# Performance work log

Hardware: AMD Instinct MI355X
Metric: run time of the kernel (lower is better)

The kernel has to match this reference:

```python
import jax, jax.numpy as jnp
import numpy as np

NUM_FRAMES = 4  # camera, person, object, world
RELATION_DIM = 14
CANONICAL_DIM = 64
BATCH = 2097152


def setup_inputs() -> dict:
    key = jax.random.key(0)
    k1, k2, k3, k4 = jax.random.split(key, 4)
    relation_logits = jax.random.normal(k1, (BATCH, RELATION_DIM), dtype=jnp.float32)
    frame_type_ids = jax.random.randint(k2, (BATCH,), 0, NUM_FRAMES, dtype=jnp.int32)
    # stacked per-frame-type Linear params: W[k] is (out=64, in=14), b[k] is (64,)
    bound = 1.0 / np.sqrt(RELATION_DIM)
    W = jax.random.uniform(k3, (NUM_FRAMES, CANONICAL_DIM, RELATION_DIM), dtype=jnp.float32,
                           minval=-bound, maxval=bound)
    b = jax.random.uniform(k4, (NUM_FRAMES, CANONICAL_DIM), dtype=jnp.float32,
                           minval=-bound, maxval=bound)
    return {"relation_logits": relation_logits, "frame_type_ids": frame_type_ids,
            "W": W, "b": b}


def reference(relation_logits, frame_type_ids, W, b):
    # Per-frame-type linear routing: out[i] = x[i] @ W[id_i].T + b[id_i].
    # Loop over the 4 small experts (fixed structural set), masked-select outputs.
    batch = relation_logits.shape[0]
    out = jnp.zeros((batch, W.shape[1]), dtype=relation_logits.dtype)
    for k in range(W.shape[0]):
        yk = relation_logits @ W[k].T + b[k]          # (batch, canonical_dim)
        sel = (frame_type_ids == k)[:, None]
        out = jnp.where(sel, yk, out)
    return out
```

## Files before the change

### kernel.cpp

```cpp
#include <hip/hip_runtime.h>
#include <stdint.h>

#define RDIM 14
#define CDIM 64
#define NFRAMES 4

constexpr int BLOCK = 256;
constexpr int TILE_ROWS = 256;
constexpr int ROWS_PER_WAVE = 64;
constexpr int X_TILE_BYTES = TILE_ROWS * RDIM * 4;
constexpr int CHUNK_BYTES  = 64 * 16;
constexpr int N_CHUNKS     = X_TILE_BYTES / CHUNK_BYTES;

typedef const __attribute__((address_space(1))) uint32_t* gptr_t;
typedef __attribute__((address_space(3))) uint32_t* lptr_t;

__global__ __launch_bounds__(BLOCK, 4) void frame_proj_kernel(
    const float* __restrict__ X,
    const int* __restrict__ ids,
    const float* __restrict__ W,
    const float* __restrict__ B,
    float* __restrict__ out,
    int batch)
{
    __shared__ float xs_lds[TILE_ROWS * RDIM];

    const int tid  = threadIdx.x;
    const int lane = tid & 63;
    const int wid  = __builtin_amdgcn_readfirstlane(tid >> 6);

    const int tileBase = blockIdx.x * TILE_ROWS;
    const int tileRows = min(TILE_ROWS, batch - tileBase);

    const int waveRow0 = wid * ROWS_PER_WAVE;
    const int gRow0    = tileBase + waveRow0;
    int idv = 0;
    if (gRow0 + lane < batch) idv = ids[gRow0 + lane];

    if (tileRows == TILE_ROWS) {
        const char* gsrc = (const char*)(X + (size_t)tileBase * RDIM);
        for (int c = wid; c < N_CHUNKS; c += 4) {
            __builtin_amdgcn_global_load_lds(
                (gptr_t)(const void*)(gsrc + c * CHUNK_BYTES + lane * 16),
                (lptr_t)(void*)((char*)xs_lds + c * CHUNK_BYTES),
                16, 0, 0);
        }
    } else {
        for (int i = tid; i < tileRows * RDIM; i += BLOCK)
            xs_lds[i] = X[(size_t)tileBase * RDIM + i];
    }

    float w[NFRAMES][RDIM];
    float bb[NFRAMES];
#pragma unroll
    for (int e = 0; e < NFRAMES; ++e) {
#pragma unroll
        for (int k = 0; k < RDIM; ++k)
            w[e][k] = W[(e * CDIM + lane) * RDIM + k];
        bb[e] = B[e * CDIM + lane];
    }
#pragma unroll
    for (int e = 0; e < NFRAMES; ++e) {
#pragma unroll
        for (int k = 0; k < RDIM; ++k)
            asm volatile("" : "+v"(w[e][k]));
        asm volatile("" : "+v"(bb[e]));
    }

    __syncthreads();

    const int nrows = min(ROWS_PER_WAVE, tileRows - waveRow0);
    const float2* xr = (const float2*)xs_lds + waveRow0 * (RDIM / 2);
    float* orow = out + (size_t)gRow0 * CDIM + lane;

    for (int r = 0; r < nrows; ++r) {
        const int id = __builtin_amdgcn_readlane(idv, r);

        float xv[RDIM];
#pragma unroll
        for (int k = 0; k < RDIM / 2; ++k) {
            float2 v = xr[r * (RDIM / 2) + k];
            xv[2 * k]     = v.x;
            xv[2 * k + 1] = v.y;
        }

        auto dot = [&](const float (&wk)[RDIM], float bias) {
            float a0 = bias, a1 = 0.0f;
#pragma unroll
            for (int k = 0; k < RDIM; k += 2) {
                a0 = fmaf(xv[k],     wk[k],     a0);
                a1 = fmaf(xv[k + 1], wk[k + 1], a1);
            }
            return a0 + a1;
        };

        float acc;
        if (id == 0)      acc = dot(w[0], bb[0]);
        else if (id == 1) acc = dot(w[1], bb[1]);
        else if (id == 2) acc = dot(w[2], bb[2]);
        else              acc = dot(w[3], bb[3]);

        orow[(size_t)r * CDIM] = acc;
    }
}

extern "C" void kernel_launch(void* const* d_in, const int* in_sizes, int n_in,
                              void* d_out, int out_size, void* d_ws, size_t ws_size,
                              hipStream_t stream) {
    const float* X   = (const float*)d_in[0];
    const int*   ids = (const int*)d_in[1];
    const float* W   = (const float*)d_in[2];
    const float* B   = (const float*)d_in[3];
    float* out = (float*)d_out;

    const int batch = in_sizes[1];

    const int grid = (batch + TILE_ROWS - 1) / TILE_ROWS;
    frame_proj_kernel<<<grid, BLOCK, 0, stream>>>(X, ids, W, B, out, batch);
}
```

Before: 617.3 us.

## Double tile rows and pad LDS rows to 16 floats for float4 reads

Tile size grows from 256 to 512 rows, so each wave handles 128 rows and needs two id registers. Each 14-float input row is now staged into a 16-float padded slot in LDS using per-lane 16-byte global_load_lds chunks, which lets the inner loop read a row with four float4 LDS loads instead of seven float2 loads. The full-tile loop is also unrolled by two. The intent is to cut LDS instruction count and amortize the weight loads over more rows. The risk is that the 16-byte chunks past float 14 read into the next row's data, which is why the fast path now requires a following tile to exist, and the larger LDS footprint reduces occupancy.

```diff
diff --git a/kernel.cpp b/kernel.cpp
--- a/kernel.cpp
+++ b/kernel.cpp
@@ -6,11 +6,13 @@
 #define NFRAMES 4
 
 constexpr int BLOCK = 256;
-constexpr int TILE_ROWS = 256;
-constexpr int ROWS_PER_WAVE = 64;
-constexpr int X_TILE_BYTES = TILE_ROWS * RDIM * 4;
-constexpr int CHUNK_BYTES  = 64 * 16;
-constexpr int N_CHUNKS     = X_TILE_BYTES / CHUNK_BYTES;
+constexpr int TILE_ROWS = 512;
+constexpr int ROWS_PER_WAVE = TILE_ROWS / 4;
+constexpr int ROW_PAD_FLOATS = 16;
+constexpr int X_TILE_BYTES = TILE_ROWS * ROW_PAD_FLOATS * 4;
+constexpr int CHUNK_BYTES = 16;
+constexpr int N_CHUNKS = X_TILE_BYTES / CHUNK_BYTES;
+constexpr int ISSUES = N_CHUNKS / 64;
 
 typedef const __attribute__((address_space(1))) uint32_t* gptr_t;
 typedef __attribute__((address_space(3))) uint32_t* lptr_t;
@@ -23,7 +25,7 @@
     float* __restrict__ out,
     int batch)
 {
-    __shared__ float xs_lds[TILE_ROWS * RDIM];
+    __shared__ float xs_lds[TILE_ROWS * ROW_PAD_FLOATS];
 
     const int tid  = threadIdx.x;
     const int lane = tid & 63;
@@ -34,73 +36,85 @@
 
     const int waveRow0 = wid * ROWS_PER_WAVE;
     const int gRow0    = tileBase + waveRow0;
-    int idv = 0;
-    if (gRow0 + lane < batch) idv = ids[gRow0 + lane];
+    int idv0 = 0, idv1 = 0;
+    if (gRow0 + lane < batch)      idv0 = ids[gRow0 + lane];
+    if (gRow0 + 64 + lane < batch) idv1 = ids[gRow0 + 64 + lane];
 
-    if (tileRows == TILE_ROWS) {
+    if (tileBase + TILE_ROWS < batch) {
         const char* gsrc = (const char*)(X + (size_t)tileBase * RDIM);
-        for (int c = wid; c < N_CHUNKS; c += 4) {
+        for (int i = wid; i < ISSUES; i += 4) {
+            const int c = i * 64 + lane;
+            const int r = c >> 2;
+            const int q = c & 3;
             __builtin_amdgcn_global_load_lds(
-                (gptr_t)(const void*)(gsrc + c * CHUNK_BYTES + lane * 16),
-                (lptr_t)(void*)((char*)xs_lds + c * CHUNK_BYTES),
+                (gptr_t)(const void*)(gsrc + r * 56 + q * 16),
+                (lptr_t)(void*)((char*)xs_lds + i * 1024),
                 16, 0, 0);
         }
     } else {
-        for (int i = tid; i < tileRows * RDIM; i += BLOCK)
-            xs_lds[i] = X[(size_t)tileBase * RDIM + i];
+        for (int i = tid; i < tileRows * ROW_PAD_FLOATS; i += BLOCK) {
+            const int r = i >> 4, k = i & 15;
+            xs_lds[i] = (k < RDIM) ? X[(size_t)(tileBase + r) * RDIM + k] : 0.0f;
+        }
     }
 
-    float w[NFRAMES][RDIM];
-    float bb[NFRAMES];
+    float2 w2[NFRAMES][7];
+    float  bb[NFRAMES];
 #pragma unroll
     for (int e = 0; e < NFRAMES; ++e) {
+        const float2* wr = (const float2*)(W + (size_t)(e * CDIM + lane) * RDIM);
 #pragma unroll
-        for (int k = 0; k < RDIM; ++k)
-            w[e][k] = W[(e * CDIM + lane) * RDIM + k];
+        for (int k = 0; k < 7; ++k) w2[e][k] = wr[k];
         bb[e] = B[e * CDIM + lane];
     }
 #pragma unroll
     for (int e = 0; e < NFRAMES; ++e) {
 #pragma unroll
-        for (int k = 0; k < RDIM; ++k)
-            asm volatile("" : "+v"(w[e][k]));
+        for (int k = 0; k < 7; ++k) asm volatile("" : "+v"(w2[e][k]));
         asm volatile("" : "+v"(bb[e]));
     }
 
     __syncthreads();
 
     const int nrows = min(ROWS_PER_WAVE, tileRows - waveRow0);
-    const float2* xr = (const float2*)xs_lds + waveRow0 * (RDIM / 2);
+    const float4* xr4 = (const float4*)xs_lds + (size_t)waveRow0 * 4;
     float* orow = out + (size_t)gRow0 * CDIM + lane;
 
-    for (int r = 0; r < nrows; ++r) {
-        const int id = __builtin_amdgcn_readlane(idv, r);
+    auto body = [&](int r) {
+        const int id = (r < 64) ? __builtin_amdgcn_readlane(idv0, r & 63)
+                                : __builtin_amdgcn_readlane(idv1, r & 63);
 
-        float xv[RDIM];
+        float4 v0 = xr4[r * 4 + 0];
+        float4 v1 = xr4[r * 4 + 1];
+        float4 v2 = xr4[r * 4 + 2];
+        float4 v3 = xr4[r * 4 + 3];
+        float2 x2[7] = { {v0.x, v0.y}, {v0.z, v0.w}, {v1.x, v1.y}, {v1.z, v1.w},
+                         {v2.x, v2.y}, {v2.z, v2.w}, {v3.x, v3.y} };
+
+        auto dot = [&](const float2 (&wk)[7], float bias) {
+            float ax = bias, ay = 0.0f;
 #pragma unroll
-        for (int k = 0; k < RDIM / 2; ++k) {
-            float2 v = xr[r * (RDIM / 2) + k];
-            xv[2 * k]     = v.x;
-            xv[2 * k + 1] = v.y;
-        }
-
-        auto dot = [&](const float (&wk)[RDIM], float bias) {
-            float a0 = bias, a1 = 0.0f;
-#pragma unroll
-            for (int k = 0; k < RDIM; k += 2) {
-                a0 = fmaf(xv[k],     wk[k],     a0);
-                a1 = fmaf(xv[k + 1], wk[k + 1], a1);
+            for (int k = 0; k < 7; ++k) {
+                ax = fmaf(x2[k].x, wk[k].x, ax);
+                ay = fmaf(x2[k].y, wk[k].y, ay);
             }
-            return a0 + a1;
+            return ax + ay;
         };
 
         float acc;
-        if (id == 0)      acc = dot(w[0], bb[0]);
-        else if (id == 1) acc = dot(w[1], bb[1]);
-        else if (id == 2) acc = dot(w[2], bb[2]);
-        else              acc = dot(w[3], bb[3]);
+        if (id == 0)      acc = dot(w2[0], bb[0]);
+        else if (id == 1) acc = dot(w2[1], bb[1]);
+        else if (id == 2) acc = dot(w2[2], bb[2]);
+        else              acc = dot(w2[3], bb[3]);
 
         orow[(size_t)r * CDIM] = acc;
+    };
+
+    if (nrows == ROWS_PER_WAVE) {
+#pragma unroll 2
+        for (int r = 0; r < ROWS_PER_WAVE; ++r) body(r);
+    } else {
+        for (int r = 0; r < nrows; ++r) body(r);
     }
 }
 
```

Result: slower. 675.0 us (+9.3%).

## Make projection kernel persistent with double-buffered LDS prefetch of input tiles

Applied to the files above, without the earlier changes.

The grid is capped at a fixed number of persistent blocks that loop over tiles. Each block prefetches the next tile's X rows into a second LDS buffer and loads the next ids while computing the current tile. The goal is to overlap input loads with compute and stores, and to pay the per-block weight register load only once. This doubles LDS use, which may cut occupancy, and adds a block barrier per tile. It also reads weights as float2.

```diff
diff --git a/kernel.cpp b/kernel.cpp
--- a/kernel.cpp
+++ b/kernel.cpp
@@ -8,9 +8,11 @@
 constexpr int BLOCK = 256;
 constexpr int TILE_ROWS = 256;
 constexpr int ROWS_PER_WAVE = 64;
-constexpr int X_TILE_BYTES = TILE_ROWS * RDIM * 4;
-constexpr int CHUNK_BYTES  = 64 * 16;
-constexpr int N_CHUNKS     = X_TILE_BYTES / CHUNK_BYTES;
+constexpr int X_TILE_FLOATS = TILE_ROWS * RDIM;
+constexpr int X_TILE_BYTES  = X_TILE_FLOATS * 4;
+constexpr int CHUNK_BYTES   = 64 * 16;
+constexpr int N_CHUNKS      = X_TILE_BYTES / CHUNK_BYTES;
+constexpr int PERSISTENT_BLOCKS = 1024;
 
 typedef const __attribute__((address_space(1))) uint32_t* gptr_t;
 typedef __attribute__((address_space(3))) uint32_t* lptr_t;
@@ -23,84 +25,112 @@
     float* __restrict__ out,
     int batch)
 {
-    __shared__ float xs_lds[TILE_ROWS * RDIM];
+    __shared__ float xs[2][X_TILE_FLOATS];
 
     const int tid  = threadIdx.x;
     const int lane = tid & 63;
     const int wid  = __builtin_amdgcn_readfirstlane(tid >> 6);
+    const int waveRow0 = wid * ROWS_PER_WAVE;
 
-    const int tileBase = blockIdx.x * TILE_ROWS;
-    const int tileRows = min(TILE_ROWS, batch - tileBase);
+    const int ntiles = (batch + TILE_ROWS - 1) / TILE_ROWS;
 
-    const int waveRow0 = wid * ROWS_PER_WAVE;
-    const int gRow0    = tileBase + waveRow0;
-    int idv = 0;
-    if (gRow0 + lane < batch) idv = ids[gRow0 + lane];
+    auto stage = [&](int tile, int buf) {
+        const int tb = tile * TILE_ROWS;
+        const int trows = min(TILE_ROWS, batch - tb);
+        if (trows == TILE_ROWS) {
+            const char* gsrc = (const char*)(X + (size_t)tb * RDIM);
+            for (int c = wid; c < N_CHUNKS; c += 4) {
+                __builtin_amdgcn_global_load_lds(
+                    (gptr_t)(const void*)(gsrc + c * CHUNK_BYTES + lane * 16),
+                    (lptr_t)(void*)((char*)xs[buf] + c * CHUNK_BYTES),
+                    16, 0, 0);
+            }
+        } else {
+            for (int i = tid; i < trows * RDIM; i += BLOCK)
+                xs[buf][i] = X[(size_t)tb * RDIM + i];
+        }
+    };
 
-    if (tileRows == TILE_ROWS) {
-        const char* gsrc = (const char*)(X + (size_t)tileBase * RDIM);
-        for (int c = wid; c < N_CHUNKS; c += 4) {
-            __builtin_amdgcn_global_load_lds(
-                (gptr_t)(const void*)(gsrc + c * CHUNK_BYTES + lane * 16),
-                (lptr_t)(void*)((char*)xs_lds + c * CHUNK_BYTES),
-                16, 0, 0);
-        }
-    } else {
-        for (int i = tid; i < tileRows * RDIM; i += BLOCK)
-            xs_lds[i] = X[(size_t)tileBase * RDIM + i];
-    }
+    auto load_ids = [&](int tile) -> int {
+        const int g = tile * TILE_ROWS + waveRow0 + lane;
+        return (g < batch) ? ids[g] : 0;
+    };
+
+    int t = blockIdx.x;
+    if (t >= ntiles) return;
+
+    stage(t, 0);
+    int idv = load_ids(t);
 
     float w[NFRAMES][RDIM];
     float bb[NFRAMES];
 #pragma unroll
     for (int e = 0; e < NFRAMES; ++e) {
+        const float2* wr = (const float2*)(W + (size_t)(e * CDIM + lane) * RDIM);
 #pragma unroll
-        for (int k = 0; k < RDIM; ++k)
-            w[e][k] = W[(e * CDIM + lane) * RDIM + k];
+        for (int k = 0; k < 7; ++k) {
+            float2 v = wr[k];
+            w[e][2 * k]     = v.x;
+            w[e][2 * k + 1] = v.y;
+        }
         bb[e] = B[e * CDIM + lane];
     }
 #pragma unroll
     for (int e = 0; e < NFRAMES; ++e) {
 #pragma unroll
-        for (int k = 0; k < RDIM; ++k)
-            asm volatile("" : "+v"(w[e][k]));
+        for (int k = 0; k < RDIM; ++k) asm volatile("" : "+v"(w[e][k]));
         asm volatile("" : "+v"(bb[e]));
     }
 
     __syncthreads();
 
-    const int nrows = min(ROWS_PER_WAVE, tileRows - waveRow0);
-    const float2* xr = (const float2*)xs_lds + waveRow0 * (RDIM / 2);
-    float* orow = out + (size_t)gRow0 * CDIM + lane;
+    int cur = 0;
+    while (true) {
+        const int tn = t + gridDim.x;
+        const bool havenext = (tn < ntiles);
+        if (havenext) stage(tn, cur ^ 1);
+        const int idv_next = havenext ? load_ids(tn) : 0;
 
-    for (int r = 0; r < nrows; ++r) {
-        const int id = __builtin_amdgcn_readlane(idv, r);
+        const int tb = t * TILE_ROWS;
+        const int nrows = min(ROWS_PER_WAVE, batch - tb - waveRow0);
+        const float2* xr2 = (const float2*)(xs[cur]) + waveRow0 * (RDIM / 2);
+        float* orow = out + (size_t)(tb + waveRow0) * CDIM + lane;
 
-        float xv[RDIM];
+        for (int r = 0; r < nrows; ++r) {
+            const int id = __builtin_amdgcn_readlane(idv, r);
+
+            float xv[RDIM];
 #pragma unroll
-        for (int k = 0; k < RDIM / 2; ++k) {
-            float2 v = xr[r * (RDIM / 2) + k];
-            xv[2 * k]     = v.x;
-            xv[2 * k + 1] = v.y;
+            for (int k = 0; k < RDIM / 2; ++k) {
+                float2 v = xr2[r * (RDIM / 2) + k];
+                xv[2 * k]     = v.x;
+                xv[2 * k + 1] = v.y;
+            }
+
+            auto dot = [&](const float (&wk)[RDIM], float bias) {
+                float a0 = bias, a1 = 0.0f;
+#pragma unroll
+                for (int k = 0; k < RDIM; k += 2) {
+                    a0 = fmaf(xv[k],     wk[k],     a0);
+                    a1 = fmaf(xv[k + 1], wk[k + 1], a1);
+                }
+                return a0 + a1;
+            };
+
+            float acc;
+            if (id == 0)      acc = dot(w[0], bb[0]);
+            else if (id == 1) acc = dot(w[1], bb[1]);
+            else if (id == 2) acc = dot(w[2], bb[2]);
+            else              acc = dot(w[3], bb[3]);
+
+            orow[(size_t)r * CDIM] = acc;
         }
 
-        auto dot = [&](const float (&wk)[RDIM], float bias) {
-            float a0 = bias, a1 = 0.0f;
-#pragma unroll
-            for (int k = 0; k < RDIM; k += 2) {
-                a0 = fmaf(xv[k],     wk[k],     a0);
-                a1 = fmaf(xv[k + 1], wk[k + 1], a1);
-            }
-            return a0 + a1;
-        };
-
-        float acc;
-        if (id == 0)      acc = dot(w[0], bb[0]);
-        else if (id == 1) acc = dot(w[1], bb[1]);
-        else if (id == 2) acc = dot(w[2], bb[2]);
-        else              acc = dot(w[3], bb[3]);
-
-        orow[(size_t)r * CDIM] = acc;
+        if (!havenext) break;
+        __syncthreads();
+        t = tn;
+        cur ^= 1;
+        idv = idv_next;
     }
 }
 
@@ -115,6 +145,7 @@
 
     const int batch = in_sizes[1];
 
-    const int grid = (batch + TILE_ROWS - 1) / TILE_ROWS;
+    const int ntiles = (batch + TILE_ROWS - 1) / TILE_ROWS;
+    const int grid = min(ntiles, PERSISTENT_BLOCKS);
     frame_proj_kernel<<<grid, BLOCK, 0, stream>>>(X, ids, W, B, out, batch);
 }
```

Result: slower. 658.4 us (+6.7%).
